# Performance work log

Measured on AMD Instinct MI355X. Metric: run time of the kernel, lower is better.

## Reference

```python
import jax, jax.numpy as jnp
import numpy as np

B, SE, SD, IN_DIM, D, DEPTH, H, DH, M, FF, NBINS = 8, 2048, 1024, 1280, 512, 4, 8, 64, 266, 2048, 128

def _ln(x, g, b):
    mu = x.mean(-1, keepdims=True)
    var = ((x - mu) ** 2).mean(-1, keepdims=True)
    return (x - mu) / jnp.sqrt(var + 1e-5) * g + b

def _gelu(x):
    return jax.nn.gelu(x, approximate=False)

def _sinusoidal(x, dim):
    # sinusoidal embedding of integer expression bins -> [.., dim]
    half = dim // 2
    freqs = jnp.exp(-jnp.log(10000.0) * jnp.arange(half, dtype=jnp.float32) / half)
    ang = x[..., None].astype(jnp.float32) * freqs
    return jnp.concatenate([jnp.sin(ang), jnp.cos(ang)], axis=-1)

def _split_heads(x):
    b, s, _ = x.shape
    return x.reshape(b, s, H, DH).transpose(0, 2, 1, 3)

def _merge_heads(x):
    b, h, s, d = x.shape
    return x.transpose(0, 2, 1, 3).reshape(b, s, h * d)

def _favor_attention(q, k, v, proj):
    # FAVOR+ softmax-kernel linear attention (non-causal), performer-style
    dn = DH ** -0.25
    ratio = M ** -0.5
    eps = 1e-4
    qd = jnp.einsum('bhsd,md->bhsm', q * dn, proj)
    kd = jnp.einsum('bhsd,md->bhsm', k * dn, proj)
    q_diag = 0.5 * (q ** 2).sum(-1, keepdims=True) * dn * dn
    k_diag = 0.5 * (k ** 2).sum(-1, keepdims=True) * dn * dn
    qp = ratio * (jnp.exp(qd - q_diag - jnp.max(qd, axis=-1, keepdims=True)) + eps)
    kp = ratio * (jnp.exp(kd - k_diag - jnp.max(kd)) + eps)
    k_sum = kp.sum(axis=2)                                   # [b,h,m]
    d_inv = 1.0 / jnp.einsum('bhsm,bhm->bhs', qp, k_sum)     # [b,h,s]
    kv = jnp.einsum('bhsm,bhsd->bhmd', kp, v)                # [b,h,m,d]
    return jnp.einsum('bhsm,bhmd->bhsd', qp, kv) * d_inv[..., None]

def _forward(var_input_encoder, var_input_decoder, var_W, var_b, enc_ln_g, enc_ln_b, dec_ln_g, dec_ln_b, p_ln1_g, p_ln1_b, p_Wq, p_Wk, p_Wv, p_Wo, p_bo, p_ln2_g, p_ln2_b, p_w1, p_b1, p_w2, p_b2, proj, ca_Wq, ca_Wk, ca_Wv, ca_Wo, ca_bo, cross_ln_g, cross_ln_b, ffd_w1, ffd_b1, ffd_w2, ffd_b2, out_ln_g, out_ln_b, head_W, head_b, expression_encoder):
    expr = _sinusoidal(expression_encoder, D)            # [B,SE,D]
    enc = var_input_encoder @ var_W + var_b              # [B,SE,D]
    dec = var_input_decoder @ var_W + var_b              # [B,SD,D]
    x = _ln(enc + expr, enc_ln_g, enc_ln_b)
    # Performer encoder: pre-LN self-attn (FAVOR+) + pre-LN FF, residuals
    for i in range(DEPTH):
        y = _ln(x, p_ln1_g[i], p_ln1_b[i])
        q = _split_heads(y @ p_Wq[i])
        k = _split_heads(y @ p_Wk[i])
        v = _split_heads(y @ p_Wv[i])
        x = x + (_merge_heads(_favor_attention(q, k, v, proj[i])) @ p_Wo[i] + p_bo[i])
        y = _ln(x, p_ln2_g[i], p_ln2_b[i])
        x = x + (_gelu(y @ p_w1[i] + p_b1[i]) @ p_w2[i] + p_b2[i])
    context = x
    # decoder: LN -> softmax cross-attention over encoder context
    dec = _ln(dec, dec_ln_g, dec_ln_b)
    q = _split_heads(dec @ ca_Wq)
    k = _split_heads(context @ ca_Wk)
    v = _split_heads(context @ ca_Wv)
    scores = jnp.einsum('bhqd,bhkd->bhqk', q, k) * (DH ** -0.5)
    o = _merge_heads(jnp.einsum('bhqk,bhkd->bhqd', jax.nn.softmax(scores, axis=-1), v)) @ ca_Wo + ca_bo
    out = _ln(o + dec, cross_ln_g, cross_ln_b)
    out = _gelu(out @ ffd_w1 + ffd_b1) @ ffd_w2 + ffd_b2   # note: no residual around FF (as in source)
    out = _ln(out, out_ln_g, out_ln_b)
    return out @ head_W + head_b                            # [B,SD,NBINS]

def setup_inputs() -> dict:
    key = jax.random.key(0)
    ks = iter(jax.random.split(key, 64))
    def w(shape, scale=0.02):
        return jax.random.normal(next(ks), shape, dtype=jnp.float32) * scale
    inp = {
        'var_input_encoder': jax.random.normal(next(ks), (B, SE, IN_DIM), dtype=jnp.float32),
        'var_input_decoder': jax.random.normal(next(ks), (B, SD, IN_DIM), dtype=jnp.float32),
        'expression_encoder': jax.random.randint(next(ks), (B, SE), 0, NBINS, dtype=jnp.int32),
        'var_W': w((IN_DIM, D)), 'var_b': jnp.zeros((D,), jnp.float32),
        'enc_ln_g': jnp.ones((D,), jnp.float32), 'enc_ln_b': jnp.zeros((D,), jnp.float32),
        'dec_ln_g': jnp.ones((D,), jnp.float32), 'dec_ln_b': jnp.zeros((D,), jnp.float32),
        'p_ln1_g': jnp.ones((DEPTH, D), jnp.float32), 'p_ln1_b': jnp.zeros((DEPTH, D), jnp.float32),
        'p_Wq': w((DEPTH, D, H * DH)), 'p_Wk': w((DEPTH, D, H * DH)), 'p_Wv': w((DEPTH, D, H * DH)),
        'p_Wo': w((DEPTH, H * DH, D)), 'p_bo': jnp.zeros((DEPTH, D), jnp.float32),
        'p_ln2_g': jnp.ones((DEPTH, D), jnp.float32), 'p_ln2_b': jnp.zeros((DEPTH, D), jnp.float32),
        'p_w1': w((DEPTH, D, FF)), 'p_b1': jnp.zeros((DEPTH, FF), jnp.float32),
        'p_w2': w((DEPTH, FF, D)), 'p_b2': jnp.zeros((DEPTH, D), jnp.float32),
        'proj': jax.random.normal(next(ks), (DEPTH, M, DH), dtype=jnp.float32),
        'ca_Wq': w((D, H * DH)), 'ca_Wk': w((D, H * DH)), 'ca_Wv': w((D, H * DH)),
        'ca_Wo': w((H * DH, D)), 'ca_bo': jnp.zeros((D,), jnp.float32),
        'cross_ln_g': jnp.ones((D,), jnp.float32), 'cross_ln_b': jnp.zeros((D,), jnp.float32),
        'ffd_w1': w((D, FF)), 'ffd_b1': jnp.zeros((FF,), jnp.float32),
        'ffd_w2': w((FF, D)), 'ffd_b2': jnp.zeros((D,), jnp.float32),
        'out_ln_g': jnp.ones((D,), jnp.float32), 'out_ln_b': jnp.zeros((D,), jnp.float32),
        'head_W': w((D, NBINS)), 'head_b': jnp.zeros((NBINS,), jnp.float32),
    }
    return inp

def reference(var_input_encoder, var_input_decoder, expression_encoder, var_W, var_b, enc_ln_g, enc_ln_b, dec_ln_g, dec_ln_b, p_ln1_g, p_ln1_b, p_Wq, p_Wk, p_Wv, p_Wo, p_bo, p_ln2_g, p_ln2_b, p_w1, p_b1, p_w2, p_b2, proj, ca_Wq, ca_Wk, ca_Wv, ca_Wo, ca_bo, cross_ln_g, cross_ln_b, ffd_w1, ffd_b1, ffd_w2, ffd_b2, out_ln_g, out_ln_b, head_W, head_b):
    return _forward(var_input_encoder, var_input_decoder, var_W, var_b, enc_ln_g, enc_ln_b, dec_ln_g, dec_ln_b, p_ln1_g, p_ln1_b, p_Wq, p_Wk, p_Wv, p_Wo, p_bo, p_ln2_g, p_ln2_b, p_w1, p_b1, p_w2, p_b2, proj, ca_Wq, ca_Wk, ca_Wv, ca_Wo, ca_bo, cross_ln_g, cross_ln_b, ffd_w1, ffd_b1, ffd_w2, ffd_b2, out_ln_g, out_ln_b, head_W, head_b, expression_encoder)
```

## Files before the change

### kernel.cpp

```cpp
#include <hip/hip_runtime.h>
#include <hip/hip_bf16.h>
#include <math.h>

constexpr int cB = 8, cSE = 2048, cSD = 1024, cIN = 1280, cD = 512,
              cDEPTH = 4, cH = 8, cDH = 64, cM = 266, cFF = 2048, cNB = 128;
constexpr int cMP = 288;

#define DEV __device__ __forceinline__

typedef __bf16 bf16;
typedef __attribute__((ext_vector_type(8))) __bf16 bf16x8;
typedef __attribute__((ext_vector_type(4))) __bf16 bf16x4;
typedef __attribute__((ext_vector_type(2))) __bf16 bf16x2;
typedef __attribute__((ext_vector_type(4))) float f32x4;

DEV float gelu_f(float x) { return 0.5f * x * (1.0f + erff(x * 0.70710678118654752440f)); }

DEV float wave_sum(float v) {
#pragma unroll
  for (int o = 32; o; o >>= 1) v += __shfl_xor(v, o);
  return v;
}
DEV float wave_max(float v) {
#pragma unroll
  for (int o = 32; o; o >>= 1) v = fmaxf(v, __shfl_xor(v, o));
  return v;
}

#define GL2LDS(gp, lp) __builtin_amdgcn_global_load_lds(                    \
    (const __attribute__((address_space(1))) void*)(gp),                    \
    (__attribute__((address_space(3))) void*)(lp), 16, 0, 0)

template <int OUT, int ACT, bool BIAS, bool RES>
__global__ __launch_bounds__(256) void gemm_mfma(
    const bf16* __restrict__ A, const bf16* __restrict__ Bt,
    void* __restrict__ Cv, bf16* __restrict__ Cv2,
    const float* __restrict__ bias, int M, int N, int K) {
  __shared__ bf16 As[2 * 128 * 32];
  __shared__ bf16 Bs[2 * 128 * 32];
  const int t = threadIdx.x, l = t & 63, w = t >> 6;
  const int g = l >> 4, c = l & 15;
  const int nwg = gridDim.x * gridDim.y;
  int id = blockIdx.y * gridDim.x + blockIdx.x;
  if ((nwg & 7) == 0) id = (id & 7) * (nwg >> 3) + (id >> 3);
  const int m0 = (id / gridDim.x) * 128, n0 = (id % gridDim.x) * 128;
  const int wr = (w >> 1) * 64, wc = (w & 1) * 64;
  const int srow = w * 32 + (l >> 2);
  const int scol = (l & 3) * 8;
  const bf16* gA = A + (size_t)(m0 + srow) * K + scol;
  const bf16* gB = Bt + (size_t)(n0 + srow) * K + scol;
  bf16* lA = As + w * 1024;
  bf16* lB = Bs + w * 1024;

  const f32x4 zero4 = {0.f, 0.f, 0.f, 0.f};
  f32x4 acc[4][4];
#pragma unroll
  for (int i = 0; i < 4; i++)
#pragma unroll
    for (int j = 0; j < 4; j++) acc[i][j] = zero4;

  for (int k0 = 0; k0 < K; k0 += 64) {
    GL2LDS(gA + k0, lA);
    GL2LDS(gA + (size_t)16 * K + k0, lA + 512);
    GL2LDS(gB + k0, lB);
    GL2LDS(gB + (size_t)16 * K + k0, lB + 512);
    GL2LDS(gA + k0 + 32, lA + 4096);
    GL2LDS(gA + (size_t)16 * K + k0 + 32, lA + 4096 + 512);
    GL2LDS(gB + k0 + 32, lB + 4096);
    GL2LDS(gB + (size_t)16 * K + k0 + 32, lB + 4096 + 512);
    __syncthreads();
#pragma unroll
    for (int hh = 0; hh < 2; hh++) {
      bf16x8 af[4], bfr[4];
#pragma unroll
      for (int i = 0; i < 4; i++)
        af[i] = *(const bf16x8*)(As + hh * 4096 + (wr + i * 16 + c) * 32 + g * 8);
#pragma unroll
      for (int j = 0; j < 4; j++)
        bfr[j] = *(const bf16x8*)(Bs + hh * 4096 + (wc + j * 16 + c) * 32 + g * 8);
#pragma unroll
      for (int i = 0; i < 4; i++)
#pragma unroll
        for (int j = 0; j < 4; j++)
          acc[i][j] = __builtin_amdgcn_mfma_f32_16x16x32_bf16(af[i], bfr[j], acc[i][j], 0, 0, 0);
    }
    __syncthreads();
  }
  float* Cf = (float*)Cv;
  bf16* Cb = (bf16*)Cv;
#pragma unroll
  for (int i = 0; i < 4; i++) {
    const int mb = m0 + wr + i * 16 + g * 4;
#pragma unroll
    for (int j = 0; j < 4; j++) {
      const int n = n0 + wc + j * 16 + c;
      const float bv = BIAS ? bias[n] : 0.f;
#pragma unroll
      for (int r = 0; r < 4; r++) {
        float v = acc[i][j][r] + bv;
        if (ACT == 1) v = gelu_f(v);
        if (ACT == 2) v *= 0.18033688011112042f;
        const size_t idx = (size_t)(mb + r) * N + n;
        if (OUT == 0 || OUT == 2) {
          float* cp = Cf + idx;
          if (RES) v += *cp;
          *cp = v;
          if (OUT == 2) Cv2[idx] = (bf16)v;
        } else {
          Cb[idx] = (bf16)v;
        }
      }
    }
  }
}

__global__ __launch_bounds__(256) void mega_prep(
    const float* __restrict__ Wq, const float* __restrict__ Wk,
    const float* __restrict__ Wv, const float* __restrict__ Wo,
    const float* __restrict__ w1, const float* __restrict__ w2,
    const float* __restrict__ var_W, const float* __restrict__ proj,
    const float* __restrict__ in_enc, const float* __restrict__ in_dec,
    bf16* __restrict__ WL, bf16* __restrict__ WtVar,
    bf16* __restrict__ projB4, bf16* __restrict__ encB,
    bf16* __restrict__ decB) {
  const int z = blockIdx.y, bid = blockIdx.x, t = threadIdx.x;
  if (z >= 26) {
    const float* src = (z == 26) ? in_enc : in_dec;
    bf16* dst = (z == 26) ? encB : decB;
    const int n = (z == 26) ? 16384 * 1280 : 8192 * 1280;
    int i = (bid * 256 + t) * 4;
    const int stride = 1024 * 256 * 4;
    for (; i < n; i += stride) {
      float4 v = *(const float4*)(src + i);
      bf16x4 o;
      o[0] = (bf16)v.x; o[1] = (bf16)v.y; o[2] = (bf16)v.z; o[3] = (bf16)v.w;
      *(bf16x4*)(dst + i) = o;
    }
    return;
  }
  if (z == 25) {
    const int idx = bid * 256 + t;
    if (idx < 4 * cMP * cDH) {
      const int layer = idx / (cMP * cDH), r = idx % (cMP * cDH);
      const int m = r >> 6;
      projB4[idx] = (bf16)(m < cM ? proj[(size_t)layer * cM * cDH + r] * 0.35355339059327373f : 0.f);
    }
    return;
  }
  __shared__ float tile[32][33];
  const float* W;
  bf16* dst;
  int K, N;
  if (z == 24) {
    W = var_W; dst = WtVar; K = 1280; N = 512;
  } else {
    const int layer = z / 6, mat = z % 6;
    bf16* base = WL + (size_t)layer * 3145728;
    if (mat < 4) {
      W = (mat == 0 ? Wq : mat == 1 ? Wk : mat == 2 ? Wv : Wo) + (size_t)layer * 262144;
      dst = base + mat * 262144; K = 512; N = 512;
    } else if (mat == 4) {
      W = w1 + (size_t)layer * 1048576; dst = base + 1048576; K = 512; N = 2048;
    } else {
      W = w2 + (size_t)layer * 1048576; dst = base + 2097152; K = 2048; N = 512;
    }
  }
  const int nt = N >> 5;
  if (bid >= nt * (K >> 5)) return;
  const int n0 = (bid % nt) * 32, k0 = (bid / nt) * 32;
  const int tx = t & 31, ty = t >> 5;
#pragma unroll
  for (int i = ty; i < 32; i += 8) tile[i][tx] = W[(size_t)(k0 + i) * N + n0 + tx];
  __syncthreads();
#pragma unroll
  for (int i = ty; i < 32; i += 8)
    dst[(size_t)(n0 + i) * K + k0 + tx] = (bf16)tile[tx][i];
}

__global__ __launch_bounds__(256) void mega_prep_dec(
    const float* __restrict__ caWq, const float* __restrict__ caWk,
    const float* __restrict__ caWv, const float* __restrict__ caWo,
    const float* __restrict__ fw1, const float* __restrict__ fw2,
    const float* __restrict__ hW, bf16* __restrict__ WD) {
  const int z = blockIdx.y, bid = blockIdx.x, t = threadIdx.x;
  __shared__ float tile[32][33];
  const float* W;
  bf16* dst;
  int K, N;
  if (z < 4) {
    W = (z == 0 ? caWq : z == 1 ? caWk : z == 2 ? caWv : caWo);
    dst = WD + z * 262144; K = 512; N = 512;
  } else if (z == 4) {
    W = fw1; dst = WD + 1048576; K = 512; N = 2048;
  } else if (z == 5) {
    W = fw2; dst = WD + 2097152; K = 2048; N = 512;
  } else {
    W = hW; dst = WD + 3145728; K = 512; N = 128;
  }
  const int nt = N >> 5;
  if (bid >= nt * (K >> 5)) return;
  const int n0 = (bid % nt) * 32, k0 = (bid / nt) * 32;
  const int tx = t & 31, ty = t >> 5;
#pragma unroll
  for (int i = ty; i < 32; i += 8) tile[i][tx] = W[(size_t)(k0 + i) * N + n0 + tx];
  __syncthreads();
#pragma unroll
  for (int i = ty; i < 32; i += 8)
    dst[(size_t)(n0 + i) * K + k0 + tx] = (bf16)tile[tx][i];
}

__global__ __launch_bounds__(256) void favor_prep(
    const bf16* __restrict__ QKV, const bf16* __restrict__ projB,
    bf16* __restrict__ Vt, float* __restrict__ bmax) {
  const int z = blockIdx.y, b = z >> 3, h = z & 7;
  const int t = threadIdx.x;
  const int ld = 1536;
  if (blockIdx.x < 32) {
    __shared__ bf16 tile[64][65];
    const bf16* Vh = QKV + 1024;
    const int s0 = blockIdx.x * 64;
#pragma unroll
    for (int r = t >> 3; r < 64; r += 32) {
      bf16x8 v = *(const bf16x8*)(Vh + ((size_t)b * cSE + s0 + r) * ld + h * cDH + (t & 7) * 8);
#pragma unroll
      for (int e = 0; e < 8; e++) tile[(t & 7) * 8 + e][r] = v[e];
    }
    __syncthreads();
    bf16* vz = Vt + (size_t)z * 80 * cSE;
#pragma unroll
    for (int d = t >> 3; d < 64; d += 32) {
      bf16x8 o;
#pragma unroll
      for (int e = 0; e < 8; e++) o[e] = tile[d][(t & 7) * 8 + e];
      *(bf16x8*)(vz + (size_t)d * cSE + s0 + (t & 7) * 8) = o;
    }
    const int rr = t >> 4, seg = (t & 15) * 4;
    bf16x4 ov;
    const float val = (rr == 0) ? 1.f : 0.f;
    ov[0] = (bf16)val; ov[1] = (bf16)val; ov[2] = (bf16)val; ov[3] = (bf16)val;
    *(bf16x4*)(vz + (size_t)(64 + rr) * cSE + s0 + seg) = ov;
    return;
  }
  __shared__ float sm[4];
  const bf16* Kh = QKV + 512;
  const int xb = blockIdx.x - 32;
  const int s0 = xb * 128;
  const int l = t & 63, w = t >> 6, g = l >> 4, c = l & 15;
  const int wr = (w >> 1) * 64, wcol = (w & 1) * 144;
  const f32x4 zero4 = {0.f, 0.f, 0.f, 0.f};
  f32x4 acc[4][9];
#pragma unroll
  for (int i = 0; i < 4; i++)
#pragma unroll
    for (int j = 0; j < 9; j++) acc[i][j] = zero4;
  const size_t abase = ((size_t)b * cSE + s0) * ld + h * cDH;
#pragma unroll
  for (int k0 = 0; k0 < 64; k0 += 32) {
    bf16x8 af[4];
#pragma unroll
    for (int i = 0; i < 4; i++)
      af[i] = *(const bf16x8*)(Kh + abase + (size_t)(wr + i * 16 + c) * ld + k0 + g * 8);
#pragma unroll
    for (int j = 0; j < 9; j++) {
      bf16x8 bfr = *(const bf16x8*)(projB + (wcol + j * 16 + c) * 64 + k0 + g * 8);
#pragma unroll
      for (int i = 0; i < 4; i++)
        acc[i][j] = __builtin_amdgcn_mfma_f32_16x16x32_bf16(af[i], bfr, acc[i][j], 0, 0, 0);
    }
  }
  float m = -3e38f;
#pragma unroll
  for (int i = 0; i < 4; i++)
#pragma unroll
    for (int j = 0; j < 9; j++) {
      const int mc = wcol + j * 16 + c;
      if (mc < cM) {
#pragma unroll
        for (int r = 0; r < 4; r++) m = fmaxf(m, acc[i][j][r]);
      }
    }
  m = wave_max(m);
  if (l == 0) sm[w] = m;
  __syncthreads();
  if (t == 0)
    bmax[z * 16 + xb] = fmaxf(fmaxf(sm[0], sm[1]), fmaxf(sm[2], sm[3]));
}

__global__ __launch_bounds__(256, 1) void favor_kkv(
    const bf16* __restrict__ Kh, int ld, const bf16* __restrict__ projB,
    const bf16* __restrict__ Vt, const float* __restrict__ bmax,
    float* __restrict__ part) {
  __shared__ bf16 kp[288 * 72];
  __shared__ float sm[4];
  const int z = blockIdx.y, b = z >> 3, h = z & 7;
  const int chunk = blockIdx.x;
  const int t = threadIdx.x, l = t & 63, w = t >> 6, g = l >> 4, c = l & 15;
  float gm;
  {
    float m = -1e30f;
    for (int i = t; i < 1024; i += 256) m = fmaxf(m, bmax[i]);
    m = wave_max(m);
    if (l == 0) sm[w] = m;
    __syncthreads();
    gm = fmaxf(fmaxf(sm[0], sm[1]), fmaxf(sm[2], sm[3]));
  }
  const int pr = (w >> 1) * 32;
  const int wcol = (w & 1) * 144;
  const int wm = (w & 1) * 144, wd = (w >> 1) * 32;
  const bool dden = (wd == 32);
  const float ratio = 0.061313927f;
  const f32x4 zero4 = {0.f, 0.f, 0.f, 0.f};
  f32x4 kacc[9][2], kaccx[9];
#pragma unroll
  for (int j = 0; j < 9; j++) {
    kacc[j][0] = zero4; kacc[j][1] = zero4; kaccx[j] = zero4;
  }
  const size_t kbase = (size_t)b * cSE * ld + h * cDH;
  const size_t vtz = (size_t)z * 80 * cSE;

  for (int st = 0; st < 256; st += 64) {
    const int sg = chunk * 256 + st;
    f32x4 pacc[2][9];
#pragma unroll
    for (int i = 0; i < 2; i++)
#pragma unroll
      for (int j = 0; j < 9; j++) pacc[i][j] = zero4;
    float sq[2] = {0.f, 0.f};
#pragma unroll
    for (int k0 = 0; k0 < 64; k0 += 32) {
      bf16x8 af[2];
#pragma unroll
      for (int i = 0; i < 2; i++) {
        af[i] = *(const bf16x8*)(Kh + kbase + (size_t)(sg + pr + i * 16 + c) * ld + k0 + g * 8);
#pragma unroll
        for (int e = 0; e < 8; e++) {
          const float v = (float)af[i][e];
          sq[i] += v * v;
        }
      }
#pragma unroll
      for (int j = 0; j < 9; j++) {
        bf16x8 bfr = *(const bf16x8*)(projB + (wcol + j * 16 + c) * 64 + k0 + g * 8);
        pacc[0][j] = __builtin_amdgcn_mfma_f32_16x16x32_bf16(af[0], bfr, pacc[0][j], 0, 0, 0);
        pacc[1][j] = __builtin_amdgcn_mfma_f32_16x16x32_bf16(af[1], bfr, pacc[1][j], 0, 0, 0);
      }
    }
#pragma unroll
    for (int i = 0; i < 2; i++) {
      sq[i] += __shfl_xor(sq[i], 16);
      sq[i] += __shfl_xor(sq[i], 32);
    }
    float rowsub[2][4];
#pragma unroll
    for (int i = 0; i < 2; i++)
#pragma unroll
      for (int r = 0; r < 4; r++)
        rowsub[i][r] = gm + 0.0625f * __shfl(sq[i], g * 4 + r);
    __syncthreads();
#pragma unroll
    for (int i = 0; i < 2; i++)
#pragma unroll
      for (int j = 0; j < 9; j++) {
        const int mc = wcol + j * 16 + c;
        bf16x4 o;
#pragma unroll
        for (int r = 0; r < 4; r++) {
          const float v = (mc < cM)
              ? ratio * (__expf(pacc[i][j][r] - rowsub[i][r]) + 1e-4f) : 0.f;
          o[r] = (bf16)v;
        }
        *(bf16x4*)(kp + (size_t)mc * 72 + pr + i * 16 + g * 4) = o;
      }
    __syncthreads();
#pragma unroll
    for (int k0 = 0; k0 < 64; k0 += 32) {
      bf16x8 bv0 = *(const bf16x8*)(Vt + vtz + (size_t)(wd + c) * cSE + sg + k0 + g * 8);
      bf16x8 bv1 = *(const bf16x8*)(Vt + vtz + (size_t)(wd + 16 + c) * cSE + sg + k0 + g * 8);
      bf16x8 bvx;
      if (dden)
        bvx = *(const bf16x8*)(Vt + vtz + (size_t)(64 + c) * cSE + sg + k0 + g * 8);
#pragma unroll
      for (int j = 0; j < 9; j++) {
        bf16x8 am = *(const bf16x8*)(kp + (size_t)(wm + j * 16 + c) * 72 + k0 + g * 8);
        kacc[j][0] = __builtin_amdgcn_mfma_f32_16x16x32_bf16(am, bv0, kacc[j][0], 0, 0, 0);
        kacc[j][1] = __builtin_amdgcn_mfma_f32_16x16x32_bf16(am, bv1, kacc[j][1], 0, 0, 0);
        if (dden)
          kaccx[j] = __builtin_amdgcn_mfma_f32_16x16x32_bf16(am, bvx, kaccx[j], 0, 0, 0);
      }
    }
  }
  float* po = part + ((size_t)z * 8 + chunk) * (cMP * 80);
#pragma unroll
  for (int j = 0; j < 9; j++)
#pragma unroll
    for (int i = 0; i < 2; i++)
#pragma unroll
      for (int r = 0; r < 4; r++)
        po[(size_t)(wm + j * 16 + g * 4 + r) * 80 + wd + i * 16 + c] = kacc[j][i][r];
  if (dden) {
#pragma unroll
    for (int j = 0; j < 9; j++)
#pragma unroll
      for (int r = 0; r < 4; r++)
        po[(size_t)(wm + j * 16 + g * 4 + r) * 80 + 64 + c] = kaccx[j][r];
  }
}

__global__ __launch_bounds__(256) void kv_reduce(
    const float* __restrict__ part, bf16* __restrict__ kvT) {
  const int z = blockIdx.y, q = blockIdx.x;
  const float* p = part + (size_t)z * 8 * (cMP * 80);
  bf16* o = kvT + (size_t)z * 80 * cMP;
  const int lo = q * 5760, hi = lo + 5760;
  for (int idx = lo + threadIdx.x; idx < hi; idx += 256) {
    const int m = idx / 80, d = idx - m * 80;
    float s = 0.f;
#pragma unroll
    for (int cc = 0; cc < 8; cc++) s += p[idx + (size_t)cc * (cMP * 80)];
    o[(size_t)d * cMP + m] = (bf16)s;
  }
}

__global__ __launch_bounds__(256, 1) void favor_qout(
    const bf16* __restrict__ Qh, int ld, const bf16* __restrict__ projB,
    const bf16* __restrict__ kvT, bf16* __restrict__ Y) {
  __shared__ bf16 Plds[128 * 296];
  __shared__ float rmaxs[4][64];
  __shared__ float denl[128];
  const int z = blockIdx.y, b = z >> 3, h = z & 7;
  const int s0 = blockIdx.x * 128;
  const int t = threadIdx.x, l = t & 63, w = t >> 6, g = l >> 4, c = l & 15;
  const int wr = (w >> 1) * 64, wcol = (w & 1) * 144;
  const f32x4 zero4 = {0.f, 0.f, 0.f, 0.f};
  f32x4 acc[4][9];
#pragma unroll
  for (int i = 0; i < 4; i++)
#pragma unroll
    for (int j = 0; j < 9; j++) acc[i][j] = zero4;
  float sq[4] = {0.f, 0.f, 0.f, 0.f};
  const size_t abase = ((size_t)b * cSE + s0) * ld + h * cDH;
#pragma unroll
  for (int k0 = 0; k0 < 64; k0 += 32) {
    bf16x8 af[4];
#pragma unroll
    for (int i = 0; i < 4; i++) {
      af[i] = *(const bf16x8*)(Qh + abase + (size_t)(wr + i * 16 + c) * ld + k0 + g * 8);
#pragma unroll
      for (int e = 0; e < 8; e++) {
        const float v = (float)af[i][e];
        sq[i] += v * v;
      }
    }
#pragma unroll
    for (int j = 0; j < 9; j++) {
      bf16x8 bfr = *(const bf16x8*)(projB + (wcol + j * 16 + c) * 64 + k0 + g * 8);
#pragma unroll
      for (int i = 0; i < 4; i++)
        acc[i][j] = __builtin_amdgcn_mfma_f32_16x16x32_bf16(af[i], bfr, acc[i][j], 0, 0, 0);
    }
  }
#pragma unroll
  for (int i = 0; i < 4; i++) {
    sq[i] += __shfl_xor(sq[i], 16);
    sq[i] += __shfl_xor(sq[i], 32);
  }
  const float ratio = 0.061313927f;
  float rowsub[4][4];
#pragma unroll
  for (int i = 0; i < 4; i++)
#pragma unroll
    for (int r = 0; r < 4; r++) {
      float m = -3e38f;
#pragma unroll
      for (int j = 0; j < 9; j++) {
        const int mc = wcol + j * 16 + c;
        m = (mc < cM) ? fmaxf(m, acc[i][j][r]) : m;
      }
      m = fmaxf(m, __shfl_xor(m, 1));
      m = fmaxf(m, __shfl_xor(m, 2));
      m = fmaxf(m, __shfl_xor(m, 4));
      m = fmaxf(m, __shfl_xor(m, 8));
      rowsub[i][r] = m;
    }
  if (c == 0) {
#pragma unroll
    for (int i = 0; i < 4; i++)
#pragma unroll
      for (int r = 0; r < 4; r++) rmaxs[w][i * 16 + g * 4 + r] = rowsub[i][r];
  }
  __syncthreads();
#pragma unroll
  for (int i = 0; i < 4; i++)
#pragma unroll
    for (int r = 0; r < 4; r++) {
      const int row = i * 16 + g * 4 + r;
      rowsub[i][r] = fmaxf(rowsub[i][r], rmaxs[w ^ 1][row]) +
                     0.0625f * __shfl(sq[i], g * 4 + r);
    }
#pragma unroll
  for (int i = 0; i < 4; i++)
#pragma unroll
    for (int j = 0; j < 9; j++) {
      const int mc = wcol + j * 16 + c;
#pragma unroll
      for (int r = 0; r < 4; r++) {
        const float v = (mc < cM)
            ? ratio * (__expf(acc[i][j][r] - rowsub[i][r]) + 1e-4f) : 0.f;
        Plds[(wr + i * 16 + g * 4 + r) * 296 + mc] = (bf16)v;
      }
    }
  __syncthreads();

  const int wd = (w & 1) * 32;
  const bool dden = (wd == 32);
  f32x4 acc2[4][2], accx[4];
#pragma unroll
  for (int i = 0; i < 4; i++) {
    acc2[i][0] = zero4; acc2[i][1] = zero4; accx[i] = zero4;
  }
  const size_t kz = (size_t)z * 80 * cMP;
#pragma unroll 3
  for (int k0 = 0; k0 < cMP; k0 += 32) {
    bf16x8 bv[2], bvx;
#pragma unroll
    for (int j = 0; j < 2; j++)
      bv[j] = *(const bf16x8*)(kvT + kz + (size_t)(wd + j * 16 + c) * cMP + k0 + g * 8);
    if (dden)
      bvx = *(const bf16x8*)(kvT + kz + (size_t)(64 + c) * cMP + k0 + g * 8);
#pragma unroll
    for (int i = 0; i < 4; i++) {
      bf16x8 av = *(const bf16x8*)(Plds + (wr + i * 16 + c) * 296 + k0 + g * 8);
      acc2[i][0] = __builtin_amdgcn_mfma_f32_16x16x32_bf16(av, bv[0], acc2[i][0], 0, 0, 0);
      acc2[i][1] = __builtin_amdgcn_mfma_f32_16x16x32_bf16(av, bv[1], acc2[i][1], 0, 0, 0);
      if (dden)
        accx[i] = __builtin_amdgcn_mfma_f32_16x16x32_bf16(av, bvx, accx[i], 0, 0, 0);
    }
  }
  if (dden && c == 0) {
#pragma unroll
    for (int i = 0; i < 4; i++)
#pragma unroll
      for (int r = 0; r < 4; r++)
        denl[wr + i * 16 + g * 4 + r] = accx[i][r];
  }
  __syncthreads();
#pragma unroll
  for (int i = 0; i < 4; i++)
#pragma unroll
    for (int r = 0; r < 4; r++) {
      const int row = wr + i * 16 + g * 4 + r;
      const float inv = 1.0f / denl[row];
#pragma unroll
      for (int j = 0; j < 2; j++)
        Y[((size_t)b * cSE + s0 + row) * cD + h * cDH + wd + j * 16 + c] =
            (bf16)(acc2[i][j][r] * inv);
    }
}

template <bool ADD, bool WF, bool WB>
__global__ __launch_bounds__(256) void ln_rows(
    const float* __restrict__ in, const float* __restrict__ add,
    const float* __restrict__ g, const float* __restrict__ be,
    float* __restrict__ out, bf16* __restrict__ out2) {
  const int wid = blockIdx.x * 4 + (threadIdx.x >> 6);
  const int lane = threadIdx.x & 63;
  const float* ip = in + (size_t)wid * cD + lane * 8;
  float x[8];
  {
    float4 a = *(const float4*)ip;
    float4 b4 = *(const float4*)(ip + 4);
    x[0] = a.x; x[1] = a.y; x[2] = a.z; x[3] = a.w;
    x[4] = b4.x; x[5] = b4.y; x[6] = b4.z; x[7] = b4.w;
  }
  if (ADD) {
    const float* ap = add + (size_t)wid * cD + lane * 8;
    float4 a = *(const float4*)ap;
    float4 b4 = *(const float4*)(ap + 4);
    x[0] += a.x; x[1] += a.y; x[2] += a.z; x[3] += a.w;
    x[4] += b4.x; x[5] += b4.y; x[6] += b4.z; x[7] += b4.w;
  }
  float s = 0;
#pragma unroll
  for (int i = 0; i < 8; i++) s += x[i];
  s = wave_sum(s);
  const float mu = s * (1.0f / cD);
  float vs = 0;
#pragma unroll
  for (int i = 0; i < 8; i++) { const float d = x[i] - mu; vs += d * d; }
  vs = wave_sum(vs);
  const float rstd = 1.0f / sqrtf(vs * (1.0f / cD) + 1e-5f);
  float r[8];
#pragma unroll
  for (int i = 0; i < 8; i++) {
    const int d = lane * 8 + i;
    r[i] = (x[i] - mu) * rstd * g[d] + be[d];
  }
  if (WF) {
    float* op = out + (size_t)wid * cD + lane * 8;
    float4 a, b4;
    a.x = r[0]; a.y = r[1]; a.z = r[2]; a.w = r[3];
    b4.x = r[4]; b4.y = r[5]; b4.z = r[6]; b4.w = r[7];
    *(float4*)op = a; *(float4*)(op + 4) = b4;
  }
  if (WB) {
    bf16x8 ov;
#pragma unroll
    for (int i = 0; i < 8; i++) ov[i] = (bf16)r[i];
    *(bf16x8*)(out2 + (size_t)wid * cD + lane * 8) = ov;
  }
}

__global__ __launch_bounds__(256) void embed_ln(
    float* __restrict__ X, const int* __restrict__ ids,
    const float* __restrict__ g, const float* __restrict__ be) {
  const int wid = blockIdx.x * 4 + (threadIdx.x >> 6);
  const int lane = threadIdx.x & 63;
  const float idv = (float)ids[wid];
  float* xp = X + (size_t)wid * cD + lane * 8;
  float x[8];
  {
    float4 a = *(const float4*)xp;
    float4 b4 = *(const float4*)(xp + 4);
    x[0] = a.x; x[1] = a.y; x[2] = a.z; x[3] = a.w;
    x[4] = b4.x; x[5] = b4.y; x[6] = b4.z; x[7] = b4.w;
  }
  const float kf = -0.03597789207803197f;
#pragma unroll
  for (int i = 0; i < 8; i++) {
    const int d = lane * 8 + i;
    float e;
    if (d < 256) e = sinf(idv * expf(kf * (float)d));
    else         e = cosf(idv * expf(kf * (float)(d - 256)));
    x[i] += e;
  }
  float s = 0;
#pragma unroll
  for (int i = 0; i < 8; i++) s += x[i];
  s = wave_sum(s);
  const float mu = s * (1.0f / cD);
  float vs = 0;
#pragma unroll
  for (int i = 0; i < 8; i++) { const float d = x[i] - mu; vs += d * d; }
  vs = wave_sum(vs);
  const float rstd = 1.0f / sqrtf(vs * (1.0f / cD) + 1e-5f);
#pragma unroll
  for (int i = 0; i < 8; i++) {
    const int d = lane * 8 + i;
    xp[i] = (x[i] - mu) * rstd * g[d] + be[d];
  }
}

__global__ __launch_bounds__(256) void flash_mfma(
    const bf16* __restrict__ Q, const bf16* __restrict__ Kc,
    const bf16* __restrict__ Vc, bf16* __restrict__ O, int ldkv) {
  __shared__ __align__(16) bf16 KP[4 * 16 * 136];
  __shared__ __align__(16) bf16 Vs[80 * 136];
  const int id = blockIdx.x;
  const int b = (id & 63) >> 3, h = id & 7, qb = id >> 6;
  const int t = threadIdx.x, l = t & 63, w = t >> 6, g = l >> 4, c = l & 15;
  const int q0 = qb * 64 + w * 16;
  bf16x8 aq[2];
  {
    const bf16* qp = Q + ((size_t)b * cSD + q0 + c) * cD + h * cDH + g * 8;
    aq[0] = *(const bf16x8*)qp;
    aq[1] = *(const bf16x8*)(qp + 32);
  }
  for (int idx = t; idx < 16 * 136; idx += 256) {
    const int rr = idx / 136, cc = idx - rr * 136;
    Vs[(64 + rr) * 136 + cc] = (bf16)(rr == 0 ? 1.f : 0.f);
  }
  const f32x4 zero4 = {0.f, 0.f, 0.f, 0.f};
  f32x4 o5[5];
#pragma unroll
  for (int j = 0; j < 5; j++) o5[j] = zero4;
  float mrow[4];
#pragma unroll
  for (int r = 0; r < 4; r++) mrow[r] = -1e30f;

  const int kr = t >> 1, kof = (t & 1) * 32;
  const int sidx = t & 31, dseg = t >> 5;
  const size_t kvbase = (size_t)b * cSE * ldkv + h * cDH;
  char* KsC = (char*)KP;
  bf16* Pw = KP + w * 16 * 136;
  const float T2 = 11.541560327111708f;

  bf16x8 pk[4], pv[4];
  auto LOADR = [&](int kt) {
    const bf16* kp = Kc + kvbase + (size_t)(kt + kr) * ldkv + kof;
#pragma unroll
    for (int i = 0; i < 4; i++) pk[i] = *(const bf16x8*)(kp + i * 8);
    const bf16* vp = Vc + kvbase + (size_t)(kt + 4 * sidx) * ldkv + dseg * 8;
#pragma unroll
    for (int i = 0; i < 4; i++) pv[i] = *(const bf16x8*)(vp + (size_t)i * ldkv);
  };
  auto WRITEL = [&]() {
    const int sw = (kr & 7) << 4;
#pragma unroll
    for (int i = 0; i < 4; i++)
      *(bf16x8*)(KsC + kr * 128 + (((kof + i * 8) * 2) ^ sw)) = pk[i];
#pragma unroll
    for (int e = 0; e < 8; e++) {
      bf16x4 q4;
      q4[0] = pv[0][e]; q4[1] = pv[1][e]; q4[2] = pv[2][e]; q4[3] = pv[3][e];
      *(bf16x4*)(Vs + (dseg * 8 + e) * 136 + 4 * sidx) = q4;
    }
  };
  LOADR(0);
  WRITEL();

  for (int kt = 0; kt < cSE; kt += 128) {
    const bool more = (kt + 128 < cSE);
    if (more) LOADR(kt + 128);
    __syncthreads();
    f32x4 s4[8];
#pragma unroll
    for (int t2 = 0; t2 < 8; t2++) {
      const int kr2 = t2 * 16 + c;
      const int sw2 = (kr2 & 7) << 4;
      bf16x8 bk0 = *(const bf16x8*)(KsC + kr2 * 128 + ((g * 16) ^ sw2));
      bf16x8 bk1 = *(const bf16x8*)(KsC + kr2 * 128 + ((64 + g * 16) ^ sw2));
      f32x4 z = zero4;
      z = __builtin_amdgcn_mfma_f32_16x16x32_bf16(aq[0], bk0, z, 0, 0, 0);
      z = __builtin_amdgcn_mfma_f32_16x16x32_bf16(aq[1], bk1, z, 0, 0, 0);
      s4[t2] = z;
    }
    __syncthreads();
#pragma unroll
    for (int r = 0; r < 4; r++) {
      float xv[8];
#pragma unroll
      for (int t2 = 0; t2 < 8; t2++) xv[t2] = s4[t2][r];
      float tm = xv[0];
#pragma unroll
      for (int t2 = 1; t2 < 8; t2++) tm = fmaxf(tm, xv[t2]);
      tm = fmaxf(tm, __shfl_xor(tm, 1));
      tm = fmaxf(tm, __shfl_xor(tm, 2));
      tm = fmaxf(tm, __shfl_xor(tm, 4));
      tm = fmaxf(tm, __shfl_xor(tm, 8));
      if (tm > mrow[r] + T2) {
        const float corr = exp2f(mrow[r] - tm);
        mrow[r] = tm;
#pragma unroll
        for (int j = 0; j < 5; j++) o5[j][r] *= corr;
      }
      const float m = mrow[r];
      const int qr = g * 4 + r;
#pragma unroll
      for (int t2 = 0; t2 < 8; t2++)
        Pw[qr * 136 + t2 * 16 + c] = (bf16)exp2f(xv[t2] - m);
    }
    bf16x8 pa[4];
#pragma unroll
    for (int ks = 0; ks < 4; ks++)
      pa[ks] = *(const bf16x8*)(Pw + c * 136 + ks * 32 + g * 8);
#pragma unroll
    for (int j = 0; j < 5; j++) {
#pragma unroll
      for (int ks = 0; ks < 4; ks++) {
        bf16x8 bv = *(const bf16x8*)(Vs + (j * 16 + c) * 136 + ks * 32 + g * 8);
        o5[j] = __builtin_amdgcn_mfma_f32_16x16x32_bf16(pa[ks], bv, o5[j], 0, 0, 0);
      }
    }
    __syncthreads();
    if (more) WRITEL();
  }
#pragma unroll
  for (int r = 0; r < 4; r++) {
    const float den = __shfl(o5[4][r], l & 48);
    const float inv = 1.0f / den;
    const size_t row = (size_t)b * cSD + q0 + g * 4 + r;
#pragma unroll
    for (int j = 0; j < 4; j++)
      O[row * cD + h * cDH + j * 16 + c] = (bf16)(o5[j][r] * inv);
  }
}

extern "C" void kernel_launch(void* const* d_in, const int* in_sizes, int n_in,
                              void* d_out, int out_size, void* d_ws, size_t ws_size,
                              hipStream_t stream) {
  const float* in_enc = (const float*)d_in[0];
  const float* in_dec = (const float*)d_in[1];
  const int* expr = (const int*)d_in[2];
  const float* var_W = (const float*)d_in[3];
  const float* var_b = (const float*)d_in[4];
  const float* enc_g = (const float*)d_in[5];
  const float* enc_b = (const float*)d_in[6];
  const float* dec_g = (const float*)d_in[7];
  const float* dec_b = (const float*)d_in[8];
  const float* ln1_g = (const float*)d_in[9];
  const float* ln1_b = (const float*)d_in[10];
  const float* Wq = (const float*)d_in[11];
  const float* Wk = (const float*)d_in[12];
  const float* Wv = (const float*)d_in[13];
  const float* Wo = (const float*)d_in[14];
  const float* bo = (const float*)d_in[15];
  const float* ln2_g = (const float*)d_in[16];
  const float* ln2_b = (const float*)d_in[17];
  const float* w1 = (const float*)d_in[18];
  const float* b1 = (const float*)d_in[19];
  const float* w2 = (const float*)d_in[20];
  const float* b2 = (const float*)d_in[21];
  const float* proj = (const float*)d_in[22];
  const float* caWq = (const float*)d_in[23];
  const float* caWk = (const float*)d_in[24];
  const float* caWv = (const float*)d_in[25];
  const float* caWo = (const float*)d_in[26];
  const float* cabo = (const float*)d_in[27];
  const float* crg = (const float*)d_in[28];
  const float* crb = (const float*)d_in[29];
  const float* fw1 = (const float*)d_in[30];
  const float* fb1 = (const float*)d_in[31];
  const float* fw2 = (const float*)d_in[32];
  const float* fb2 = (const float*)d_in[33];
  const float* og = (const float*)d_in[34];
  const float* ob = (const float*)d_in[35];
  const float* hW = (const float*)d_in[36];
  const float* hb = (const float*)d_in[37];

  float* X     = (float*)d_ws;
  float* DC    = X + 8388608;
  bf16*  QKV   = (bf16*)(DC + 4194304);
  bf16*  Vt    = QKV + 25165824;
  bf16*  Pb    = Vt + 10485760;
  float* part  = (float*)(Pb + 50331648);
  bf16*  kvT   = (bf16*)(part + 11796480);
  float* bmax  = (float*)(kvT + 1474560);
  bf16*  Yb    = (bf16*)(bmax + 1040);
  bf16*  DCb   = Yb + 8388608;
  bf16*  Wt    = DCb + 4194304;
  bf16*  projB4 = Wt + 1048576;
  const size_t need_bytes = (size_t)75458576 * 4;
  if (ws_size < need_bytes) return;

  bf16* encB = Pb;
  bf16* decB = (bf16*)part;
  bf16* Pmid = Pb;
  bf16* WL   = Pb + 33554432;
  bf16* Xb   = Vt;
  bf16* Qc   = Pb + 8388608;
  bf16* KVc  = Pb + 12582912;
  bf16* Fb   = Pb + 29360128;
  bf16* Pm2  = Pb + 33554432;
  bf16* WD   = (bf16*)part;

  const dim3 blk(256);

  mega_prep<<<dim3(1024, 28), blk, 0, stream>>>(Wq, Wk, Wv, Wo, w1, w2, var_W, proj,
                                                in_enc, in_dec, WL, Wt, projB4,
                                                encB, decB);
  gemm_mfma<0, 0, true, false><<<dim3(4, 128), blk, 0, stream>>>(encB, Wt, X, nullptr, var_b, 16384, 512, 1280);
  gemm_mfma<0, 0, true, false><<<dim3(4, 64), blk, 0, stream>>>(decB, Wt, DC, nullptr, var_b, 8192, 512, 1280);
  embed_ln<<<4096, blk, 0, stream>>>(X, expr, enc_g, enc_b);
  ln_rows<false, true, true><<<2048, blk, 0, stream>>>(DC, nullptr, dec_g, dec_b, DC, DCb);

  for (int i = 0; i < cDEPTH; i++) {
    bf16* Wl = WL + (size_t)i * 3145728;
    bf16* projB = projB4 + (size_t)i * (cMP * cDH);
    ln_rows<false, false, true><<<4096, blk, 0, stream>>>(X, nullptr, ln1_g + i * cD, ln1_b + i * cD, nullptr, Yb);
    gemm_mfma<1, 0, false, false><<<dim3(12, 128), blk, 0, stream>>>(Yb, Wl, QKV, nullptr, nullptr, 16384, 1536, 512);
    favor_prep<<<dim3(48, 64), blk, 0, stream>>>(QKV, projB, Vt, bmax);
    favor_kkv<<<dim3(8, 64), blk, 0, stream>>>(QKV + 512, 1536, projB, Vt, bmax, part);
    kv_reduce<<<dim3(4, 64), blk, 0, stream>>>(part, kvT);
    favor_qout<<<dim3(16, 64), blk, 0, stream>>>(QKV, 1536, projB, kvT, Yb);
    gemm_mfma<0, 0, true, true><<<dim3(4, 128), blk, 0, stream>>>(Yb, Wl + 786432, X, nullptr, bo + i * cD, 16384, 512, 512);
    ln_rows<false, false, true><<<4096, blk, 0, stream>>>(X, nullptr, ln2_g + i * cD, ln2_b + i * cD, nullptr, Yb);
    gemm_mfma<1, 1, true, false><<<dim3(16, 128), blk, 0, stream>>>(Yb, Wl + 1048576, Pmid, nullptr, b1 + i * cFF, 16384, 2048, 512);
    if (i < cDEPTH - 1) {
      gemm_mfma<0, 0, true, true><<<dim3(4, 128), blk, 0, stream>>>(Pmid, Wl + 2097152, X, nullptr, b2 + i * cD, 16384, 512, 2048);
    } else {
      gemm_mfma<2, 0, true, true><<<dim3(4, 128), blk, 0, stream>>>(Pmid, Wl + 2097152, X, Xb, b2 + i * cD, 16384, 512, 2048);
    }
  }

  mega_prep_dec<<<dim3(1024, 7), blk, 0, stream>>>(caWq, caWk, caWv, caWo, fw1, fw2, hW, WD);
  gemm_mfma<1, 2, false, false><<<dim3(4, 64), blk, 0, stream>>>(DCb, WD, Qc, nullptr, nullptr, 8192, 512, 512);
  gemm_mfma<1, 0, false, false><<<dim3(8, 128), blk, 0, stream>>>(Xb, WD + 262144, KVc, nullptr, nullptr, 16384, 1024, 512);
  flash_mfma<<<dim3(1024), blk, 0, stream>>>(Qc, KVc, KVc + 512, Fb, 1024);
  gemm_mfma<0, 0, true, false><<<dim3(4, 64), blk, 0, stream>>>(Fb, WD + 786432, X, nullptr, cabo, 8192, 512, 512);
  ln_rows<true, false, true><<<2048, blk, 0, stream>>>(X, DC, crg, crb, nullptr, Yb);
  gemm_mfma<1, 1, true, false><<<dim3(16, 64), blk, 0, stream>>>(Yb, WD + 1048576, Pm2, nullptr, fb1, 8192, 2048, 512);
  gemm_mfma<0, 0, true, false><<<dim3(4, 64), blk, 0, stream>>>(Pm2, WD + 2097152, X + 4194304, nullptr, fb2, 8192, 512, 2048);
  ln_rows<false, false, true><<<2048, blk, 0, stream>>>(X + 4194304, nullptr, og, ob, nullptr, Yb);
  gemm_mfma<0, 0, true, false><<<dim3(1, 64), blk, 0, stream>>>(Yb, WD + 3145728, (float*)d_out, nullptr, hb, 8192, 128, 512);
}
```

Measured before the change: 1.932 ms.

## Store residual stream and decoder activations in bf16, add MFMA priority hints

Result: faster. 1.850 ms (-4.2%).

```diff
diff --git a/kernel.cpp b/kernel.cpp
--- a/kernel.cpp
+++ b/kernel.cpp
@@ -101,11 +101,14 @@
         if (ACT == 1) v = gelu_f(v);
         if (ACT == 2) v *= 0.18033688011112042f;
         const size_t idx = (size_t)(mb + r) * N + n;
-        if (OUT == 0 || OUT == 2) {
+        if (OUT == 0) {
           float* cp = Cf + idx;
           if (RES) v += *cp;
           *cp = v;
-          if (OUT == 2) Cv2[idx] = (bf16)v;
+        } else if (OUT == 3) {
+          bf16* cp = Cb + idx;
+          v += (float)*cp;
+          *cp = (bf16)v;
         } else {
           Cb[idx] = (bf16)v;
         }
@@ -557,27 +560,21 @@
     }
 }
 
-template <bool ADD, bool WF, bool WB>
-__global__ __launch_bounds__(256) void ln_rows(
-    const float* __restrict__ in, const float* __restrict__ add,
+template <bool ADD>
+__global__ __launch_bounds__(256) void ln_rows_b(
+    const bf16* __restrict__ in, const bf16* __restrict__ add,
     const float* __restrict__ g, const float* __restrict__ be,
-    float* __restrict__ out, bf16* __restrict__ out2) {
+    bf16* __restrict__ out) {
   const int wid = blockIdx.x * 4 + (threadIdx.x >> 6);
   const int lane = threadIdx.x & 63;
-  const float* ip = in + (size_t)wid * cD + lane * 8;
+  bf16x8 iv = *(const bf16x8*)(in + (size_t)wid * cD + lane * 8);
   float x[8];
-  {
-    float4 a = *(const float4*)ip;
-    float4 b4 = *(const float4*)(ip + 4);
-    x[0] = a.x; x[1] = a.y; x[2] = a.z; x[3] = a.w;
-    x[4] = b4.x; x[5] = b4.y; x[6] = b4.z; x[7] = b4.w;
-  }
+#pragma unroll
+  for (int i = 0; i < 8; i++) x[i] = (float)iv[i];
   if (ADD) {
-    const float* ap = add + (size_t)wid * cD + lane * 8;
-    float4 a = *(const float4*)ap;
-    float4 b4 = *(const float4*)(ap + 4);
-    x[0] += a.x; x[1] += a.y; x[2] += a.z; x[3] += a.w;
-    x[4] += b4.x; x[5] += b4.y; x[6] += b4.z; x[7] += b4.w;
+    bf16x8 av = *(const bf16x8*)(add + (size_t)wid * cD + lane * 8);
+#pragma unroll
+    for (int i = 0; i < 8; i++) x[i] += (float)av[i];
   }
   float s = 0;
 #pragma unroll
@@ -589,41 +586,26 @@
   for (int i = 0; i < 8; i++) { const float d = x[i] - mu; vs += d * d; }
   vs = wave_sum(vs);
   const float rstd = 1.0f / sqrtf(vs * (1.0f / cD) + 1e-5f);
-  float r[8];
+  bf16x8 ov;
 #pragma unroll
   for (int i = 0; i < 8; i++) {
     const int d = lane * 8 + i;
-    r[i] = (x[i] - mu) * rstd * g[d] + be[d];
-  }
-  if (WF) {
-    float* op = out + (size_t)wid * cD + lane * 8;
-    float4 a, b4;
-    a.x = r[0]; a.y = r[1]; a.z = r[2]; a.w = r[3];
-    b4.x = r[4]; b4.y = r[5]; b4.z = r[6]; b4.w = r[7];
-    *(float4*)op = a; *(float4*)(op + 4) = b4;
-  }
-  if (WB) {
-    bf16x8 ov;
-#pragma unroll
-    for (int i = 0; i < 8; i++) ov[i] = (bf16)r[i];
-    *(bf16x8*)(out2 + (size_t)wid * cD + lane * 8) = ov;
-  }
-}
-
-__global__ __launch_bounds__(256) void embed_ln(
-    float* __restrict__ X, const int* __restrict__ ids,
+    ov[i] = (bf16)((x[i] - mu) * rstd * g[d] + be[d]);
+  }
+  *(bf16x8*)(out + (size_t)wid * cD + lane * 8) = ov;
+}
+
+__global__ __launch_bounds__(256) void embed_ln_b(
+    bf16* __restrict__ X, const int* __restrict__ ids,
     const float* __restrict__ g, const float* __restrict__ be) {
   const int wid = blockIdx.x * 4 + (threadIdx.x >> 6);
   const int lane = threadIdx.x & 63;
   const float idv = (float)ids[wid];
-  float* xp = X + (size_t)wid * cD + lane * 8;
+  bf16* xp = X + (size_t)wid * cD + lane * 8;
+  bf16x8 iv = *(const bf16x8*)xp;
   float x[8];
-  {
-    float4 a = *(const float4*)xp;
-    float4 b4 = *(const float4*)(xp + 4);
-    x[0] = a.x; x[1] = a.y; x[2] = a.z; x[3] = a.w;
-    x[4] = b4.x; x[5] = b4.y; x[6] = b4.z; x[7] = b4.w;
-  }
+#pragma unroll
+  for (int i = 0; i < 8; i++) x[i] = (float)iv[i];
   const float kf = -0.03597789207803197f;
 #pragma unroll
   for (int i = 0; i < 8; i++) {
@@ -643,11 +625,13 @@
   for (int i = 0; i < 8; i++) { const float d = x[i] - mu; vs += d * d; }
   vs = wave_sum(vs);
   const float rstd = 1.0f / sqrtf(vs * (1.0f / cD) + 1e-5f);
+  bf16x8 ov;
 #pragma unroll
   for (int i = 0; i < 8; i++) {
     const int d = lane * 8 + i;
-    xp[i] = (x[i] - mu) * rstd * g[d] + be[d];
-  }
+    ov[i] = (bf16)((x[i] - mu) * rstd * g[d] + be[d]);
+  }
+  *(bf16x8*)xp = ov;
 }
 
 __global__ __launch_bounds__(256) void flash_mfma(
@@ -713,6 +697,7 @@
     if (more) LOADR(kt + 128);
     __syncthreads();
     f32x4 s4[8];
+    __builtin_amdgcn_s_setprio(1);
 #pragma unroll
     for (int t2 = 0; t2 < 8; t2++) {
       const int kr2 = t2 * 16 + c;
@@ -724,6 +709,7 @@
       z = __builtin_amdgcn_mfma_f32_16x16x32_bf16(aq[1], bk1, z, 0, 0, 0);
       s4[t2] = z;
     }
+    __builtin_amdgcn_s_setprio(0);
     __syncthreads();
 #pragma unroll
     for (int r = 0; r < 4; r++) {
@@ -753,6 +739,7 @@
 #pragma unroll
     for (int ks = 0; ks < 4; ks++)
       pa[ks] = *(const bf16x8*)(Pw + c * 136 + ks * 32 + g * 8);
+    __builtin_amdgcn_s_setprio(1);
 #pragma unroll
     for (int j = 0; j < 5; j++) {
 #pragma unroll
@@ -761,6 +748,7 @@
         o5[j] = __builtin_amdgcn_mfma_f32_16x16x32_bf16(pa[ks], bv, o5[j], 0, 0, 0);
       }
     }
+    __builtin_amdgcn_s_setprio(0);
     __syncthreads();
     if (more) WRITEL();
   }
@@ -817,9 +805,11 @@
   const float* hW = (const float*)d_in[36];
   const float* hb = (const float*)d_in[37];
 
-  float* X     = (float*)d_ws;
-  float* DC    = X + 8388608;
-  bf16*  QKV   = (bf16*)(DC + 4194304);
+  float* base  = (float*)d_ws;
+  bf16*  Xr    = (bf16*)base;
+  bf16*  Dt1   = Xr + 8388608;
+  bf16*  Dt2   = Dt1 + 4194304;
+  bf16*  QKV   = (bf16*)(base + 12582912);
   bf16*  Vt    = QKV + 25165824;
   bf16*  Pb    = Vt + 10485760;
   float* part  = (float*)(Pb + 50331648);
@@ -836,7 +826,6 @@
   bf16* decB = (bf16*)part;
   bf16* Pmid = Pb;
   bf16* WL   = Pb + 33554432;
-  bf16* Xb   = Vt;
   bf16* Qc   = Pb + 8388608;
   bf16* KVc  = Pb + 12582912;
   bf16* Fb   = Pb + 29360128;
@@ -848,38 +837,34 @@
   mega_prep<<<dim3(1024, 28), blk, 0, stream>>>(Wq, Wk, Wv, Wo, w1, w2, var_W, proj,
                                                 in_enc, in_dec, WL, Wt, projB4,
                                                 encB, decB);
-  gemm_mfma<0, 0, true, false><<<dim3(4, 128), blk, 0, stream>>>(encB, Wt, X, nullptr, var_b, 16384, 512, 1280);
-  gemm_mfma<0, 0, true, false><<<dim3(4, 64), blk, 0, stream>>>(decB, Wt, DC, nullptr, var_b, 8192, 512, 1280);
-  embed_ln<<<4096, blk, 0, stream>>>(X, expr, enc_g, enc_b);
-  ln_rows<false, true, true><<<2048, blk, 0, stream>>>(DC, nullptr, dec_g, dec_b, DC, DCb);
+  gemm_mfma<1, 0, true, false><<<dim3(4, 128), blk, 0, stream>>>(encB, Wt, Xr, nullptr, var_b, 16384, 512, 1280);
+  gemm_mfma<1, 0, true, false><<<dim3(4, 64), blk, 0, stream>>>(decB, Wt, Dt1, nullptr, var_b, 8192, 512, 1280);
+  embed_ln_b<<<4096, blk, 0, stream>>>(Xr, expr, enc_g, enc_b);
+  ln_rows_b<false><<<2048, blk, 0, stream>>>(Dt1, nullptr, dec_g, dec_b, DCb);
 
   for (int i = 0; i < cDEPTH; i++) {
     bf16* Wl = WL + (size_t)i * 3145728;
     bf16* projB = projB4 + (size_t)i * (cMP * cDH);
-    ln_rows<false, false, true><<<4096, blk, 0, stream>>>(X, nullptr, ln1_g + i * cD, ln1_b + i * cD, nullptr, Yb);
+    ln_rows_b<false><<<4096, blk, 0, stream>>>(Xr, nullptr, ln1_g + i * cD, ln1_b + i * cD, Yb);
     gemm_mfma<1, 0, false, false><<<dim3(12, 128), blk, 0, stream>>>(Yb, Wl, QKV, nullptr, nullptr, 16384, 1536, 512);
     favor_prep<<<dim3(48, 64), blk, 0, stream>>>(QKV, projB, Vt, bmax);
     favor_kkv<<<dim3(8, 64), blk, 0, stream>>>(QKV + 512, 1536, projB, Vt, bmax, part);
     kv_reduce<<<dim3(4, 64), blk, 0, stream>>>(part, kvT);
     favor_qout<<<dim3(16, 64), blk, 0, stream>>>(QKV, 1536, projB, kvT, Yb);
-    gemm_mfma<0, 0, true, true><<<dim3(4, 128), blk, 0, stream>>>(Yb, Wl + 786432, X, nullptr, bo + i * cD, 16384, 512, 512);
-    ln_rows<false, false, true><<<4096, blk, 0, stream>>>(X, nullptr, ln2_g + i * cD, ln2_b + i * cD, nullptr, Yb);
+    gemm_mfma<3, 0, true, false><<<dim3(4, 128), blk, 0, stream>>>(Yb, Wl + 786432, Xr, nullptr, bo + i * cD, 16384, 512, 512);
+    ln_rows_b<false><<<4096, blk, 0, stream>>>(Xr, nullptr, ln2_g + i * cD, ln2_b + i * cD, Yb);
     gemm_mfma<1, 1, true, false><<<dim3(16, 128), blk, 0, stream>>>(Yb, Wl + 1048576, Pmid, nullptr, b1 + i * cFF, 16384, 2048, 512);
-    if (i < cDEPTH - 1) {
-      gemm_mfma<0, 0, true, true><<<dim3(4, 128), blk, 0, stream>>>(Pmid, Wl + 2097152, X, nullptr, b2 + i * cD, 16384, 512, 2048);
-    } else {
-      gemm_mfma<2, 0, true, true><<<dim3(4, 128), blk, 0, stream>>>(Pmid, Wl + 2097152, X, Xb, b2 + i * cD, 16384, 512, 2048);
-    }
+    gemm_mfma<3, 0, true, false><<<dim3(4, 128), blk, 0, stream>>>(Pmid, Wl + 2097152, Xr, nullptr, b2 + i * cD, 16384, 512, 2048);
   }
 
   mega_prep_dec<<<dim3(1024, 7), blk, 0, stream>>>(caWq, caWk, caWv, caWo, fw1, fw2, hW, WD);
   gemm_mfma<1, 2, false, false><<<dim3(4, 64), blk, 0, stream>>>(DCb, WD, Qc, nullptr, nullptr, 8192, 512, 512);
-  gemm_mfma<1, 0, false, false><<<dim3(8, 128), blk, 0, stream>>>(Xb, WD + 262144, KVc, nullptr, nullptr, 16384, 1024, 512);
+  gemm_mfma<1, 0, false, false><<<dim3(8, 128), blk, 0, stream>>>(Xr, WD + 262144, KVc, nullptr, nullptr, 16384, 1024, 512);
   flash_mfma<<<dim3(1024), blk, 0, stream>>>(Qc, KVc, KVc + 512, Fb, 1024);
-  gemm_mfma<0, 0, true, false><<<dim3(4, 64), blk, 0, stream>>>(Fb, WD + 786432, X, nullptr, cabo, 8192, 512, 512);
-  ln_rows<true, false, true><<<2048, blk, 0, stream>>>(X, DC, crg, crb, nullptr, Yb);
+  gemm_mfma<1, 0, true, false><<<dim3(4, 64), blk, 0, stream>>>(Fb, WD + 786432, Dt1, nullptr, cabo, 8192, 512, 512);
+  ln_rows_b<true><<<2048, blk, 0, stream>>>(Dt1, DCb, crg, crb, Yb);
   gemm_mfma<1, 1, true, false><<<dim3(16, 64), blk, 0, stream>>>(Yb, WD + 1048576, Pm2, nullptr, fb1, 8192, 2048, 512);
-  gemm_mfma<0, 0, true, false><<<dim3(4, 64), blk, 0, stream>>>(Pm2, WD + 2097152, X + 4194304, nullptr, fb2, 8192, 512, 2048);
-  ln_rows<false, false, true><<<2048, blk, 0, stream>>>(X + 4194304, nullptr, og, ob, nullptr, Yb);
+  gemm_mfma<1, 0, true, false><<<dim3(4, 64), blk, 0, stream>>>(Pm2, WD + 2097152, Dt2, nullptr, fb2, 8192, 512, 2048);
+  ln_rows_b<false><<<2048, blk, 0, stream>>>(Dt2, nullptr, og, ob, Yb);
   gemm_mfma<0, 0, true, false><<<dim3(1, 64), blk, 0, stream>>>(Yb, WD + 3145728, (float*)d_out, nullptr, hb, 8192, 128, 512);
 }
```
